# Optimization experiments

Hardware: AMD Instinct MI355X
Metric: run time of the kernel (lower is better)

Reference implementation:

```python
import jax, jax.numpy as jnp
import numpy as np

ALPHA = 0.1

def ewma(y, alpha=ALPHA):
    # y: [B, T, D]; x_ewma[0] = y[0], x_ewma[t] = alpha*y[t] + (1-alpha)*x_ewma[t-1]
    y_t = jnp.swapaxes(y, 0, 1)  # [T, B, D]
    def step(carry, xt):
        c = alpha * xt + (1.0 - alpha) * carry
        return c, c
    _, out = jax.lax.scan(step, y_t[0], y_t[1:])  # [T-1, B, D]
    out = jnp.concatenate([y_t[:1], out], axis=0)  # [T, B, D]
    return jnp.swapaxes(out, 0, 1)


def setup_inputs() -> dict:
    key = jax.random.key(0)
    k1, k2, k3, k4, k5 = jax.random.split(key, 5)
    B, C, T, D = 32, 32, 2048, 512
    x = jax.random.normal(k1, (B, C, T), dtype=jnp.float32)
    W_ve = jax.random.normal(k2, (D, C), dtype=jnp.float32) * (1.0 / np.sqrt(C))
    b_ve = jax.random.normal(k3, (D,), dtype=jnp.float32) * 0.01
    W_lin = jax.random.normal(k4, (D, D), dtype=jnp.float32) * (1.0 / np.sqrt(D))
    b_lin = jax.random.normal(k5, (D,), dtype=jnp.float32) * 0.01
    return {"x": x, "W_ve": W_ve, "b_ve": b_ve, "W_lin": W_lin, "b_lin": b_lin}


def reference(x, W_ve, b_ve, W_lin, b_lin):
    # x: [B, C, T] -> [B, T, C]
    xt = jnp.transpose(x, (0, 2, 1))
    B, T, C = xt.shape
    # first-difference with leading zero row
    x_diff = jnp.concatenate(
        [jnp.zeros((B, 1, C), dtype=xt.dtype), xt[:, 1:, :] - xt[:, :-1, :]], axis=1
    )
    # value embedding: Linear(C -> D)
    x_emb = jnp.einsum("btc,dc->btd", x_diff, W_ve) + b_ve
    # bidirectional EWMA smoothing
    x_lr = ewma(x_emb)
    x_rl = jnp.flip(ewma(jnp.flip(x_emb, axis=1)), axis=1)
    x_smooth = (x_lr + x_rl) * 0.5
    # output projection: Linear(D -> D)
    return jnp.einsum("btd,ed->bte", x_smooth, W_lin) + b_lin
```

## Files before the change

kernel.cpp:

```cpp
#include <hip/hip_runtime.h>

constexpr int B = 32, C = 32, T = 2048, D = 512;
constexpr float ALPHA = 0.1f;
constexpr float BETA  = 0.9f;
constexpr float LOG2_BETA = -0.15200309344504997f;
constexpr float BETA16    = 0.18530201888518410f;

typedef float floatx4 __attribute__((ext_vector_type(4)));

constexpr int CHUNK = 128;
constexpr int SUB   = 16;
constexpr int NSUB  = CHUNK / SUB;
constexpr int LEAD  = 132;
constexpr int WIN   = LEAD + CHUNK + 128;
constexpr int PAD   = WIN + 2;

__global__ __launch_bounds__(256) void combine_weights(
    const float* __restrict__ W_ve, const float* __restrict__ b_ve,
    const float* __restrict__ W_lin, const float* __restrict__ b_lin,
    float* __restrict__ W_comb, float* __restrict__ b_comb) {
  int e  = blockIdx.x;
  int c  = threadIdx.x & 31;
  int ds = threadIdx.x >> 5;
  float acc = 0.f, accb = 0.f;
#pragma unroll 4
  for (int i = 0; i < 64; ++i) {
    int d = ds * 64 + i;
    float wl = W_lin[e * D + d];
    acc  += wl * W_ve[d * C + c];
    accb += wl * b_ve[d];
  }
  __shared__ float red[8][33];
  __shared__ float redb[8];
  red[ds][c] = acc;
  if (c == 0) redb[ds] = accb;
  __syncthreads();
  if (ds == 0) {
    float ssum = 0.f;
#pragma unroll
    for (int k = 0; k < 8; ++k) ssum += red[k][c];
    W_comb[e * C + c] = ssum;
    if (c == 0) {
      float sb = 0.f;
#pragma unroll
      for (int k = 0; k < 8; ++k) sb += redb[k];
      b_comb[e] = sb + b_lin[e];
    }
  }
}

__global__ __launch_bounds__(256) void fused_main(
    const float* __restrict__ x, const float* __restrict__ W_comb,
    const float* __restrict__ b_comb, float* __restrict__ out) {
  int b   = blockIdx.y;
  int t0  = blockIdx.x * CHUNK;
  int wlo = t0 - LEAD;

  __shared__ float xl[C * PAD];
  __shared__ float Lf[2][NSUB][C];
  __shared__ float Lb[2][NSUB][C];
  const float* xb = x + (size_t)b * C * T;

  int c   = threadIdx.x & 31;
  int sub = threadIdx.x >> 5;

  float dlast = xb[c * T + (T - 1)] - xb[c * T + (T - 2)];

  if (wlo >= 0 && wlo + WIN <= T) {
    for (int idx = threadIdx.x; idx < C * (WIN / 4); idx += 256) {
      int cc = idx / (WIN / 4);
      int q  = idx - cc * (WIN / 4);
      float4 v   = *(const float4*)(xb + cc * T + wlo + 4 * q);
      float* dst = xl + cc * PAD + 4 * q;
      ((float2*)dst)[0] = make_float2(v.x, v.y);
      ((float2*)dst)[1] = make_float2(v.z, v.w);
    }
  } else {
    for (int idx = threadIdx.x; idx < C * WIN; idx += 256) {
      int cc = idx / WIN;
      int tt = idx - cc * WIN;
      int t  = min(max(wlo + tt, 0), T - 1);
      xl[cc * PAD + tt] = xb[cc * T + t];
    }
  }

  int li   = threadIdx.x & 127;
  int half = threadIdx.x >> 7;
  int e0   = li * 4;
  float w[4][C], bias[4];
#pragma unroll
  for (int j = 0; j < 4; ++j) {
    const float4* wr = (const float4*)(W_comb + (e0 + j) * C);
#pragma unroll
    for (int c4 = 0; c4 < C / 4; ++c4) {
      float4 wv = wr[c4];
      w[j][c4 * 4 + 0] = wv.x;
      w[j][c4 * 4 + 1] = wv.y;
      w[j][c4 * 4 + 2] = wv.z;
      w[j][c4 * 4 + 3] = wv.w;
    }
    bias[j] = b_comb[e0 + j];
  }
  __syncthreads();

  int ts = t0 + sub * SUB;
  const float* xc = xl + c * PAD - wlo;
#define DD(t) (xc[(t)] - xc[(t) - 1])

  int ha = t0 - 128   + sub * SUB;
  int ba = t0 + CHUNK + sub * SUB;
  float fh = 0.f, bh = 0.f;
#pragma unroll
  for (int i = 0; i < SUB; ++i) {
    fh = ALPHA * DD(ha + i)           + BETA * fh;
    bh = ALPHA * DD(ba + SUB - 1 - i) + BETA * bh;
  }
  float lr[SUB], rl[SUB];
  float fm = 0.f, bm = 0.f;
#pragma unroll
  for (int i = 0; i < SUB; ++i) {
    fm = ALPHA * DD(ts + i) + BETA * fm;
    lr[i] = fm;
    bm = ALPHA * DD(ts + SUB - 1 - i) + BETA * bm;
    rl[SUB - 1 - i] = bm;
  }
  Lf[0][sub][c] = fh;
  Lf[1][sub][c] = lr[SUB - 1];
  Lb[0][sub][c] = bh;
  Lb[1][sub][c] = rl[0];
  __syncthreads();
#undef DD

  float Cc = 0.f, Bc = 0.f;
#pragma unroll
  for (int h = 0; h < NSUB; ++h) {
    Cc = BETA16 * Cc + Lf[0][h][c];
    Bc = BETA16 * Bc + Lb[0][NSUB - 1 - h][c];
  }
#pragma unroll
  for (int j = 0; j < NSUB - 1; ++j) {
    float cn = BETA16 * Cc + Lf[1][j][c];
    float bn = BETA16 * Bc + Lb[1][NSUB - 1 - j][c];
    Cc = (j < sub)            ? cn : Cc;
    Bc = (NSUB - 1 - j > sub) ? bn : Bc;
  }
  float f = BETA * Cc;
#pragma unroll
  for (int i = 0; i < SUB; ++i) { lr[i] += f; f *= BETA; }
  float g = BETA * Bc;
  float e = exp2f((float)(T - ts - (SUB - 1)) * LOG2_BETA);
#pragma unroll
  for (int i = SUB - 1; i >= 0; --i) {
    lr[i] = 0.5f * (lr[i] + (rl[i] + g) + e * dlast);
    g *= BETA;
    e *= BETA;
  }

  float* sbuf = xl;
  {
    int tbase = sub * SUB;
#pragma unroll
    for (int i = 0; i < SUB; ++i) sbuf[(tbase + i) * C + c] = lr[i];
  }
  __syncthreads();

  const float* srow = sbuf + half * (CHUNK / 2) * C;
  float* orow = out + ((size_t)b * T + t0 + half * (CHUNK / 2)) * D + e0;

#pragma unroll 2
  for (int t = 0; t < CHUNK / 2; ++t) {
    float a[4], a2[4];
#pragma unroll
    for (int j = 0; j < 4; ++j) { a[j] = bias[j]; a2[j] = 0.f; }
    const float4* sr4 = (const float4*)(srow + t * C);
#pragma unroll
    for (int c4 = 0; c4 < C / 4; ++c4) {
      float4 sv = sr4[c4];
      int cc = c4 * 4;
#pragma unroll
      for (int j = 0; j < 4; ++j) {
        a[j]  += sv.x * w[j][cc + 0];
        a2[j] += sv.y * w[j][cc + 1];
        a[j]  += sv.z * w[j][cc + 2];
        a2[j] += sv.w * w[j][cc + 3];
      }
    }
    floatx4 o;
    o.x = a[0] + a2[0];
    o.y = a[1] + a2[1];
    o.z = a[2] + a2[2];
    o.w = a[3] + a2[3];
    __builtin_nontemporal_store(o, (floatx4*)(orow + (size_t)t * D));
  }
}

extern "C" void kernel_launch(void* const* d_in, const int* in_sizes, int n_in,
                              void* d_out, int out_size, void* d_ws, size_t ws_size,
                              hipStream_t stream) {
  const float* x     = (const float*)d_in[0];
  const float* W_ve  = (const float*)d_in[1];
  const float* b_ve  = (const float*)d_in[2];
  const float* W_lin = (const float*)d_in[3];
  const float* b_lin = (const float*)d_in[4];
  float* out = (float*)d_out;

  float* W_comb = (float*)d_ws;
  float* b_comb = W_comb + (size_t)D * C;

  combine_weights<<<D, 256, 0, stream>>>(W_ve, b_ve, W_lin, b_lin, W_comb, b_comb);
  fused_main<<<dim3(T / CHUNK, B), 256, 0, stream>>>(x, W_comb, b_comb, out);
}
```

Measured before the change: 177.3 us.

## Stage smoothed rows in global workspace and feed GEMM via scalar loads

The smoothed 128x32 tile is now written to a global workspace instead of LDS. The output projection loop reads each row into SGPRs with double-buffered s_load_dwordx16 pairs, so the FMAs take scalar operands and the per-row LDS broadcast reads disappear. The LDS pad also changes to an odd stride, and staging stores become scalar writes to reduce bank conflicts. The risks are an extra global round trip, reliance on scalar-cache visibility of vector stores after the barrier, a prefetch two rows past the tile end, and a workspace that must be large enough.

```diff
diff --git a/kernel.cpp b/kernel.cpp
--- a/kernel.cpp
+++ b/kernel.cpp
@@ -1,4 +1,5 @@
 #include <hip/hip_runtime.h>
+#include <stdint.h>
 
 constexpr int B = 32, C = 32, T = 2048, D = 512;
 constexpr float ALPHA = 0.1f;
@@ -7,13 +8,14 @@
 constexpr float BETA16    = 0.18530201888518410f;
 
 typedef float floatx4 __attribute__((ext_vector_type(4)));
+typedef float f32x16  __attribute__((ext_vector_type(16)));
 
 constexpr int CHUNK = 128;
 constexpr int SUB   = 16;
 constexpr int NSUB  = CHUNK / SUB;
 constexpr int LEAD  = 132;
 constexpr int WIN   = LEAD + CHUNK + 128;
-constexpr int PAD   = WIN + 2;
+constexpr int PAD   = WIN + 1;
 
 __global__ __launch_bounds__(256) void combine_weights(
     const float* __restrict__ W_ve, const float* __restrict__ b_ve,
@@ -49,9 +51,20 @@
   }
 }
 
+#define SLOAD2(d0, d1, addr)                              \
+  asm volatile("s_load_dwordx16 %0, %2, 0x0\n\t"          \
+               "s_load_dwordx16 %1, %2, 0x40"             \
+               : "=&s"(d0), "=&s"(d1) : "s"(addr))
+#define SWAIT()                                           \
+  do {                                                    \
+    asm volatile("s_waitcnt lgkmcnt(0)");                 \
+    __builtin_amdgcn_sched_barrier(0);                    \
+  } while (0)
+
 __global__ __launch_bounds__(256) void fused_main(
     const float* __restrict__ x, const float* __restrict__ W_comb,
-    const float* __restrict__ b_comb, float* __restrict__ out) {
+    const float* __restrict__ b_comb, float* __restrict__ s_ws,
+    float* __restrict__ out) {
   int b   = blockIdx.y;
   int t0  = blockIdx.x * CHUNK;
   int wlo = t0 - LEAD;
@@ -60,6 +73,7 @@
   __shared__ float Lf[2][NSUB][C];
   __shared__ float Lb[2][NSUB][C];
   const float* xb = x + (size_t)b * C * T;
+  float* sblk = s_ws + ((size_t)b * (T / CHUNK) + blockIdx.x) * (CHUNK * C);
 
   int c   = threadIdx.x & 31;
   int sub = threadIdx.x >> 5;
@@ -72,8 +86,7 @@
       int q  = idx - cc * (WIN / 4);
       float4 v   = *(const float4*)(xb + cc * T + wlo + 4 * q);
       float* dst = xl + cc * PAD + 4 * q;
-      ((float2*)dst)[0] = make_float2(v.x, v.y);
-      ((float2*)dst)[1] = make_float2(v.z, v.w);
+      dst[0] = v.x; dst[1] = v.y; dst[2] = v.z; dst[3] = v.w;
     }
   } else {
     for (int idx = threadIdx.x; idx < C * WIN; idx += 256) {
@@ -156,33 +169,44 @@
     e *= BETA;
   }
 
-  float* sbuf = xl;
   {
-    int tbase = sub * SUB;
-#pragma unroll
-    for (int i = 0; i < SUB; ++i) sbuf[(tbase + i) * C + c] = lr[i];
-  }
-  __syncthreads();
-
-  const float* srow = sbuf + half * (CHUNK / 2) * C;
+    float* srw = sblk + (sub * SUB) * C + c;
+#pragma unroll
+    for (int i = 0; i < SUB; ++i) srw[i * C] = lr[i];
+  }
+  __syncthreads();
+
+  const float* srow = sblk + half * (CHUNK / 2) * C;
+  uint64_t srp_raw = (uint64_t)(uintptr_t)srow;
+  uint32_t srp_lo = __builtin_amdgcn_readfirstlane((uint32_t)srp_raw);
+  uint32_t srp_hi = __builtin_amdgcn_readfirstlane((uint32_t)(srp_raw >> 32));
+  uint64_t srp = ((uint64_t)srp_hi << 32) | srp_lo;
   float* orow = out + ((size_t)b * T + t0 + half * (CHUNK / 2)) * D + e0;
 
-#pragma unroll 2
-  for (int t = 0; t < CHUNK / 2; ++t) {
+  auto gemm_row = [&](int t, const f32x16& s0, const f32x16& s1) {
     float a[4], a2[4];
 #pragma unroll
     for (int j = 0; j < 4; ++j) { a[j] = bias[j]; a2[j] = 0.f; }
-    const float4* sr4 = (const float4*)(srow + t * C);
-#pragma unroll
-    for (int c4 = 0; c4 < C / 4; ++c4) {
-      float4 sv = sr4[c4];
-      int cc = c4 * 4;
-#pragma unroll
-      for (int j = 0; j < 4; ++j) {
-        a[j]  += sv.x * w[j][cc + 0];
-        a2[j] += sv.y * w[j][cc + 1];
-        a[j]  += sv.z * w[j][cc + 2];
-        a2[j] += sv.w * w[j][cc + 3];
+#pragma unroll
+    for (int k = 0; k < 16; ++k) {
+      float sv = s0[k];
+      if ((k & 1) == 0) {
+#pragma unroll
+        for (int j = 0; j < 4; ++j) a[j] += sv * w[j][k];
+      } else {
+#pragma unroll
+        for (int j = 0; j < 4; ++j) a2[j] += sv * w[j][k];
+      }
+    }
+#pragma unroll
+    for (int k = 0; k < 16; ++k) {
+      float sv = s1[k];
+      if ((k & 1) == 0) {
+#pragma unroll
+        for (int j = 0; j < 4; ++j) a[j] += sv * w[j][16 + k];
+      } else {
+#pragma unroll
+        for (int j = 0; j < 4; ++j) a2[j] += sv * w[j][16 + k];
       }
     }
     floatx4 o;
@@ -191,6 +215,18 @@
     o.z = a[2] + a2[2];
     o.w = a[3] + a2[3];
     __builtin_nontemporal_store(o, (floatx4*)(orow + (size_t)t * D));
+  };
+
+  f32x16 sA0, sA1, sB0, sB1;
+  SLOAD2(sA0, sA1, srp);
+#pragma unroll 1
+  for (int t = 0; t < CHUNK / 2; t += 2) {
+    SWAIT();
+    SLOAD2(sB0, sB1, srp + (uint64_t)(t + 1) * (C * 4));
+    gemm_row(t, sA0, sA1);
+    SWAIT();
+    SLOAD2(sA0, sA1, srp + (uint64_t)(t + 2) * (C * 4));
+    gemm_row(t + 1, sB0, sB1);
   }
 }
 
@@ -206,7 +242,8 @@
 
   float* W_comb = (float*)d_ws;
   float* b_comb = W_comb + (size_t)D * C;
+  float* s_ws   = b_comb + D;
 
   combine_weights<<<D, 256, 0, stream>>>(W_ve, b_ve, W_lin, b_lin, W_comb, b_comb);
-  fused_main<<<dim3(T / CHUNK, B), 256, 0, stream>>>(x, W_comb, b_comb, out);
+  fused_main<<<dim3(T / CHUNK, B), 256, 0, stream>>>(x, W_comb, b_comb, s_ws, out);
 }
```

New measurement: 218.0 us. 1.23x slower.
